# Kernel tuning notes

Measured on AMD Instinct MI355X. Metric: run time of the kernel, lower is better.

The kernel has to match this reference:

```python
import jax, jax.numpy as jnp
import numpy as np

E = 16      # num_experts
K = 2       # top-k
C = 1280    # capacity = ceil(8192*2/16*1.25)


def setup_inputs() -> dict:
    key = jax.random.key(0)
    ks = jax.random.split(key, 7)
    B, T, D, F, DFF = 4, 2048, 1024, 512, 512
    s = 0.02
    return {
        "hidden_state": jax.random.normal(ks[0], (B, T, D), jnp.float32),
        "router_w": jax.random.normal(ks[1], (D, E), jnp.float32) * s,
        "shared_gate_w": jax.random.normal(ks[2], (D, 1), jnp.float32) * s,
        "w1": jax.random.normal(ks[3], (E, D, F), jnp.float32) * s,
        "w2": jax.random.normal(ks[4], (E, F, D), jnp.float32) * s,
        "sw1": jax.random.normal(ks[5], (D, DFF), jnp.float32) * s,
        "sw2": jax.random.normal(ks[6], (DFF, D), jnp.float32) * s,
    }


def reference(hidden_state, router_w, shared_gate_w, w1, w2, sw1, sw2):
    B, T, D = hidden_state.shape
    N = B * T
    # Router: softmax over expert logits + shared sigmoid gate
    logits = jnp.einsum("btd,de->bte", hidden_state, router_w)
    scores = jax.nn.softmax(logits, axis=-1)                      # [B,T,E]
    g_shared = jax.nn.sigmoid(jnp.einsum("btd,do->bto", hidden_state, shared_gate_w))

    topk_vals, topk_idx = jax.lax.top_k(scores, K)                # [B,T,K]
    x = hidden_state.reshape(N, D)
    token_for_route = jnp.repeat(jnp.arange(N), K)                # [N*K]
    expert_for_route = topk_idx.reshape(-1)                       # [N*K]
    gate_for_route = topk_vals.reshape(-1)                        # [N*K]

    # Stable sort by expert (jnp.argsort is stable)
    order = jnp.argsort(expert_for_route)
    expert_sorted = expert_for_route[order]
    token_sorted = token_for_route[order]
    gate_sorted = gate_for_route[order]
    x_sorted = x[token_sorted]                                    # [N*K, D]

    counts = jnp.bincount(expert_sorted, length=E)
    starts = jnp.cumsum(counts) - counts
    r = jnp.arange(N * K)
    positions = r - starts[expert_sorted]                         # slot within expert
    keep = (positions < C) & (gate_sorted != 0)
    p_idx = jnp.clip(positions, 0, C - 1)

    # Scatter kept tokens into fixed-capacity buffers; dropped routes go to dummy row E
    e_safe = jnp.where(keep, expert_sorted, E)
    p_safe = jnp.where(keep, p_idx, 0)
    buf = jnp.zeros((E + 1, C, D), x.dtype).at[e_safe, p_safe].set(
        jnp.where(keep[:, None], x_sorted, 0.0)
    )
    expert_inputs = buf[:E]                                       # [E,C,D]

    # Batched expert FFN (exact GELU, matching torch default)
    h = jax.nn.gelu(jnp.einsum("ech,ehf->ecf", expert_inputs, w1), approximate=False)
    expert_outputs = jnp.einsum("ecf,efh->ech", h, w2)            # [E,C,D]

    gate_eff = jnp.where(keep, gate_sorted, 0.0)
    y_sorted = expert_outputs[expert_sorted, p_idx] * gate_eff[:, None]

    # Combine: scatter-add back to tokens
    y_out = jnp.zeros((N, D), x.dtype).at[token_sorted].add(y_sorted).reshape(B, T, D)

    # Shared expert path
    shared_out = (jax.nn.gelu(x @ sw1, approximate=False) @ sw2).reshape(B, T, D)
    y_out = y_out + g_shared * shared_out

    # Stats (no attention_mask path)
    load_counts = jnp.bincount(expert_for_route, length=E)
    load = load_counts / (load_counts.sum() + 1e-12)
    importance = scores.mean(axis=(0, 1))
    return (y_out, importance, load)
```

## Files before the change

kernel.cpp:

```cpp
#include <hip/hip_runtime.h>
#include <hip/hip_bf16.h>
#include <math.h>

#define N_TOK 8192
#define DIM 1024
#define NEXP 16
#define CAP 1280
#define FDIM 512
#define NROUTE (N_TOK * 2)
#define NCHUNK 64
#define ECAP (NEXP * CAP)
#define TOTROW (ECAP + N_TOK)

typedef __hip_bfloat16 bf16;
typedef unsigned short ushort_t;
typedef __attribute__((ext_vector_type(8))) short bf16x8;
typedef __attribute__((ext_vector_type(4))) float f32x4;

__device__ __forceinline__ float gelu_fast(float x) {
    float u = 1.5957691216057308f * (x + 0.044715f * x * x * x);
    return x / (1.f + __expf(-u));
}

__device__ __forceinline__ float bf2f(unsigned short u) {
    union { float f; unsigned int i; } v; v.i = ((unsigned int)u) << 16; return v.f;
}

__device__ __forceinline__ unsigned short f2b(float f) {
    union { __hip_bfloat16 h; unsigned short u; } v;
    v.h = __float2bfloat16(f);
    return v.u;
}

__device__ __forceinline__ void gload16(const void* g, void* l) {
    __builtin_amdgcn_global_load_lds(
        (const __attribute__((address_space(1))) unsigned int*)g,
        (__attribute__((address_space(3))) unsigned int*)l,
        16, 0, 0);
}

__device__ __forceinline__ int swz_addr16(int r, int q) {
    return ((r >> 1) << 3) + ((r & 1) << 2) + (q ^ ((r >> 1) & 3));
}

__global__ __launch_bounds__(256) void gather_x_kernel(
    const ushort_t* __restrict__ x_bf, const int* __restrict__ slot_token,
    const int* __restrict__ counts_cap, ushort_t* __restrict__ xg)
{
    int row = blockIdx.x;
    int e = row / CAP;
    int pos = row - e * CAP;
    int tok = (pos < counts_cap[e]) ? slot_token[row] : 0;
    if ((unsigned)tok >= N_TOK) tok = 0;
    int c = threadIdx.x * 4;
    ushort4 v = *reinterpret_cast<const ushort4*>(x_bf + (size_t)tok * DIM + c);
    *reinterpret_cast<ushort4*>(xg + (size_t)row * DIM + c) = v;
}

#define PREP_RTR_BLOCKS 512
#define PREP_NWG (PREP_RTR_BLOCKS + 1088)
__global__ __launch_bounds__(256) void prep_kernel(
    const float* __restrict__ x, const float* __restrict__ rw,
    const float* __restrict__ sgw,
    const float* __restrict__ w1, const float* __restrict__ w2,
    const float* __restrict__ sw1, const float* __restrict__ sw2,
    float* __restrict__ scores,
    int* __restrict__ topk_idx,
    float* __restrict__ topk_val,
    float* __restrict__ g_shared,
    ushort_t* __restrict__ x_bf,
    ushort_t* __restrict__ w1t, ushort_t* __restrict__ w2t,
    ushort_t* __restrict__ sw1t, ushort_t* __restrict__ sw2t)
{
    __shared__ union {
        ushort_t tileB[128][130];
        struct {
            float acc[4][16][4][4];
            float g[4][16];
        } r;
    } sm;

    if (blockIdx.x < PREP_RTR_BLOCKS) {
        int tid = threadIdx.x;
        int w = tid >> 6;
        int lane = tid & 63;
        int tok0 = blockIdx.x * 16;

        {
            int dq = w * 256 + lane * 4;
            float4 gv = *reinterpret_cast<const float4*>(sgw + dq);
#pragma unroll 4
            for (int tt = 0; tt < 16; ++tt) {
                const float* xr = x + (size_t)(tok0 + tt) * DIM + dq;
                float4 xv = *reinterpret_cast<const float4*>(xr);
                ushort4 o;
                o.x = f2b(xv.x); o.y = f2b(xv.y); o.z = f2b(xv.z); o.w = f2b(xv.w);
                *reinterpret_cast<ushort4*>(x_bf + (size_t)(tok0 + tt) * DIM + dq) = o;
                float dg = xv.x * gv.x + xv.y * gv.y + xv.z * gv.z + xv.w * gv.w;
#pragma unroll
                for (int m = 1; m < 64; m <<= 1) dg += __shfl_xor(dg, m, 64);
                if (lane == 0) sm.r.g[w][tt] = dg;
            }
        }

        int tok = lane >> 2;
        int e4 = lane & 3;
        int token = tok0 + tok;
        {
            const float* xr = x + (size_t)token * DIM + w * 256;
            const float* rwb = rw + (size_t)(w * 256) * NEXP + e4 * 4;
            float4 a0 = {0,0,0,0}, a1 = {0,0,0,0}, a2 = {0,0,0,0}, a3 = {0,0,0,0};
#pragma unroll 4
            for (int i = 0; i < 64; ++i) {
                float4 xv = *reinterpret_cast<const float4*>(xr + i * 4);
                const float* rp = rwb + (size_t)i * 4 * NEXP;
                float4 w0 = *reinterpret_cast<const float4*>(rp);
                float4 w1v = *reinterpret_cast<const float4*>(rp + NEXP);
                float4 w2v = *reinterpret_cast<const float4*>(rp + 2 * NEXP);
                float4 w3v = *reinterpret_cast<const float4*>(rp + 3 * NEXP);
                a0.x += xv.x * w0.x;  a0.y += xv.x * w0.y;  a0.z += xv.x * w0.z;  a0.w += xv.x * w0.w;
                a1.x += xv.y * w1v.x; a1.y += xv.y * w1v.y; a1.z += xv.y * w1v.z; a1.w += xv.y * w1v.w;
                a2.x += xv.z * w2v.x; a2.y += xv.z * w2v.y; a2.z += xv.z * w2v.z; a2.w += xv.z * w2v.w;
                a3.x += xv.w * w3v.x; a3.y += xv.w * w3v.y; a3.z += xv.w * w3v.z; a3.w += xv.w * w3v.w;
            }
            sm.r.acc[w][tok][e4][0] = (a0.x + a1.x) + (a2.x + a3.x);
            sm.r.acc[w][tok][e4][1] = (a0.y + a1.y) + (a2.y + a3.y);
            sm.r.acc[w][tok][e4][2] = (a0.z + a1.z) + (a2.z + a3.z);
            sm.r.acc[w][tok][e4][3] = (a0.w + a1.w) + (a2.w + a3.w);
        }
        __syncthreads();

        if (w != 0) return;

        float L0 = sm.r.acc[0][tok][e4][0] + sm.r.acc[1][tok][e4][0]
                 + sm.r.acc[2][tok][e4][0] + sm.r.acc[3][tok][e4][0];
        float L1 = sm.r.acc[0][tok][e4][1] + sm.r.acc[1][tok][e4][1]
                 + sm.r.acc[2][tok][e4][1] + sm.r.acc[3][tok][e4][1];
        float L2 = sm.r.acc[0][tok][e4][2] + sm.r.acc[1][tok][e4][2]
                 + sm.r.acc[2][tok][e4][2] + sm.r.acc[3][tok][e4][2];
        float L3 = sm.r.acc[0][tok][e4][3] + sm.r.acc[1][tok][e4][3]
                 + sm.r.acc[2][tok][e4][3] + sm.r.acc[3][tok][e4][3];

        float mx = fmaxf(fmaxf(L0, L1), fmaxf(L2, L3));
        mx = fmaxf(mx, __shfl_xor(mx, 1, 4));
        mx = fmaxf(mx, __shfl_xor(mx, 2, 4));
        float P0 = expf(L0 - mx), P1 = expf(L1 - mx);
        float P2 = expf(L2 - mx), P3 = expf(L3 - mx);
        float s = (P0 + P1) + (P2 + P3);
        s += __shfl_xor(s, 1, 4);
        s += __shfl_xor(s, 2, 4);
        float inv = 1.f / s;
        P0 *= inv; P1 *= inv; P2 *= inv; P3 *= inv;

        float4 Pv = {P0, P1, P2, P3};
        *reinterpret_cast<float4*>(scores + (size_t)token * NEXP + e4 * 4) = Pv;

        int base = e4 * 4;
        float v = P0; int idx = base;
        if (P1 > v) { v = P1; idx = base + 1; }
        if (P2 > v) { v = P2; idx = base + 2; }
        if (P3 > v) { v = P3; idx = base + 3; }
#pragma unroll
        for (int m = 1; m < 4; m <<= 1) {
            float vo = __shfl_xor(v, m, 4);
            int io = __shfl_xor(idx, m, 4);
            if (vo > v || (vo == v && io < idx)) { v = vo; idx = io; }
        }
        int i0 = idx; float v0 = v;
        float q0 = (base + 0 == i0) ? -1.f : P0;
        float q1 = (base + 1 == i0) ? -1.f : P1;
        float q2 = (base + 2 == i0) ? -1.f : P2;
        float q3 = (base + 3 == i0) ? -1.f : P3;
        v = q0; idx = base;
        if (q1 > v) { v = q1; idx = base + 1; }
        if (q2 > v) { v = q2; idx = base + 2; }
        if (q3 > v) { v = q3; idx = base + 3; }
#pragma unroll
        for (int m = 1; m < 4; m <<= 1) {
            float vo = __shfl_xor(v, m, 4);
            int io = __shfl_xor(idx, m, 4);
            if (vo > v || (vo == v && io < idx)) { v = vo; idx = io; }
        }
        if (e4 == 0) {
            topk_idx[2 * token] = i0; topk_idx[2 * token + 1] = idx;
            topk_val[2 * token] = v0; topk_val[2 * token + 1] = v;
            float ag = (sm.r.g[0][tok] + sm.r.g[1][tok]) + (sm.r.g[2][tok] + sm.r.g[3][tok]);
            g_shared[token] = 1.f / (1.f + expf(-ag));
        }
        return;
    }

    int bx = blockIdx.x - PREP_RTR_BLOCKS;
    const float* src; ushort_t* dst; int K, N, kt, nt;
    if (bx < 512) {
        int e = bx >> 5, r = bx & 31;
        K = 1024; N = 512; kt = r >> 2; nt = r & 3;
        src = w1 + (size_t)e * K * N; dst = w1t + (size_t)e * K * N;
    } else if (bx < 1024) {
        int b2 = bx - 512, e = b2 >> 5, r = b2 & 31;
        K = 512; N = 1024; kt = r >> 3; nt = r & 7;
        src = w2 + (size_t)e * K * N; dst = w2t + (size_t)e * K * N;
    } else if (bx < 1056) {
        int r = bx - 1024;
        K = 1024; N = 512; kt = r >> 2; nt = r & 3;
        src = sw1; dst = sw1t;
    } else {
        int r = bx - 1056;
        K = 512; N = 1024; kt = r >> 3; nt = r & 7;
        src = sw2; dst = sw2t;
    }
    int t = threadIdx.x;
#pragma unroll 4
    for (int i = 0; i < 16; ++i) {
        int u = t + 256 * i;
        int r = u >> 5;
        int c4 = (u & 31) * 4;
        float4 v = *reinterpret_cast<const float4*>(
            src + (size_t)(kt * 128 + r) * N + nt * 128 + c4);
        sm.tileB[c4 + 0][r] = f2b(v.x);
        sm.tileB[c4 + 1][r] = f2b(v.y);
        sm.tileB[c4 + 2][r] = f2b(v.z);
        sm.tileB[c4 + 3][r] = f2b(v.w);
    }
    __syncthreads();
#pragma unroll 4
    for (int i2 = 0; i2 < 8; ++i2) {
        int u = t + 256 * i2;
        int n = u >> 4;
        int kc = (u & 15) * 8;
        bf16x8 o;
#pragma unroll
        for (int j = 0; j < 8; ++j) o[j] = (short)sm.tileB[n][kc + j];
        *reinterpret_cast<bf16x8*>(dst + (size_t)(nt * 128 + n) * K + kt * 128 + kc) = o;
    }
}

__global__ __launch_bounds__(256) void hist_kernel(
    const int* __restrict__ topk_idx, int* __restrict__ chunk_hist)
{
    __shared__ int h[NEXP];
    int tid = threadIdx.x;
    if (tid < NEXP) h[tid] = 0;
    __syncthreads();
    int r = blockIdx.x * 256 + tid;
    atomicAdd(&h[topk_idx[r]], 1);
    __syncthreads();
    if (tid < NEXP) chunk_hist[blockIdx.x * NEXP + tid] = h[tid];
}

__global__ __launch_bounds__(64) void scan_kernel(
    const int* __restrict__ chunk_hist, int* __restrict__ chunk_off,
    int* __restrict__ counts_cap, float* __restrict__ out_tail)
{
    int e = threadIdx.x;
    if (e >= NEXP) return;
    int run = 0;
    for (int b = 0; b < NCHUNK; ++b) {
        chunk_off[b * NEXP + e] = run;
        run += chunk_hist[b * NEXP + e];
    }
    counts_cap[e] = run < CAP ? run : CAP;
    out_tail[NEXP + e] = (float)((double)run / 16384.0);
}

__global__ __launch_bounds__(256) void assign_kernel(
    const int* __restrict__ topk_idx, const float* __restrict__ topk_val,
    const int* __restrict__ chunk_off,
    int* __restrict__ route_slot, int* __restrict__ slot_token)
{
    __shared__ int wave_cnt[4][NEXP];
    int tid = threadIdx.x;
    int lane = tid & 63;
    int w = tid >> 6;
    int r = blockIdx.x * 256 + tid;
    int e = topk_idx[r];
    float gate = topk_val[r];
    int rank_w = 0;
#pragma unroll
    for (int e16 = 0; e16 < NEXP; ++e16) {
        unsigned long long bal = __ballot(e == e16);
        if (e == e16) rank_w = __popcll(bal & ((1ull << lane) - 1ull));
        if (lane == 0) wave_cnt[w][e16] = __popcll(bal);
    }
    __syncthreads();
    int rank = rank_w;
#pragma unroll
    for (int w2 = 0; w2 < 3; ++w2)
        if (w2 < w) rank += wave_cnt[w2][e];
    int pos = chunk_off[blockIdx.x * NEXP + e] + rank;
    int slot = -1;
    if (pos < CAP && gate != 0.f) {
        slot = e * CAP + pos;
        slot_token[slot] = r >> 1;
    }
    route_slot[r] = slot;
}

__global__ __launch_bounds__(256) void importance_kernel(
    const float* __restrict__ scores, float* __restrict__ out_tail)
{
    __shared__ float red[256];
    int e = blockIdx.x;
    float s = 0.f;
    for (int t = threadIdx.x; t < N_TOK; t += 256) s += scores[t * NEXP + e];
    red[threadIdx.x] = s;
    __syncthreads();
    for (int st = 128; st > 0; st >>= 1) {
        if (threadIdx.x < st) red[threadIdx.x] += red[threadIdx.x + st];
        __syncthreads();
    }
    if (threadIdx.x == 0) out_tail[e] = red[0] / (float)N_TOK;
}

#define G1_GX (NEXP * 5 + N_TOK / 256)
#define G1_NWG (G1_GX * (FDIM / 128))
__global__ __launch_bounds__(512) void gemm1_mfma(
    const ushort_t* __restrict__ xg,
    const ushort_t* __restrict__ x_bf,
    const ushort_t* __restrict__ w1t,
    const ushort_t* __restrict__ sw1t,
    const int* __restrict__ counts_cap,
    ushort_t* __restrict__ h_buf)
{
    __shared__ ushort_t As[3][256 * 32];
    __shared__ ushort_t Bs[3][128 * 32];

    int flat = blockIdx.x;
    int wg = (flat & 7) * (G1_NWG / 8) + (flat >> 3);
    int by = wg & 3;
    int bxg = wg >> 2;

    int g, rb;
    if (bxg < NEXP * 5) { g = bxg / 5; rb = bxg % 5; }
    else { g = NEXP; rb = bxg - NEXP * 5; }
    int Mg = (g < NEXP) ? counts_cap[g] : N_TOK;
    int m0 = rb * 256;
    if (m0 >= Mg) return;
    const ushort_t* Arows = (g < NEXP) ? (xg + ((size_t)g * CAP + m0) * DIM)
                                       : (x_bf + (size_t)m0 * DIM);
    const ushort_t* Bt = (g < NEXP) ? (w1t + (size_t)g * DIM * FDIM) : sw1t;
    int n0 = by * 128;
    int t = threadIdx.x;

    const ushort_t* asrc[2];
    const ushort_t* bsrc;
#pragma unroll
    for (int i = 0; i < 2; ++i) {
        int s = t + i * 512;
        int lr = ((s >> 3) << 1) | ((s >> 2) & 1);
        int qq = (s & 3) ^ ((s >> 3) & 3);
        asrc[i] = Arows + (size_t)lr * DIM + qq * 8;
    }
    {
        int s = t;
        int lr = ((s >> 3) << 1) | ((s >> 2) & 1);
        int qq = (s & 3) ^ ((s >> 3) & 3);
        bsrc = Bt + (size_t)(n0 + lr) * DIM + qq * 8;
    }

    int lane = t & 63;
    int w = t >> 6;
    int wm = (w & 3) * 64, wn = (w >> 2) * 64;
    int l15 = lane & 15, q = lane >> 4;

    int aoff[4], boff[4];
#pragma unroll
    for (int m = 0; m < 4; ++m) aoff[m] = swz_addr16(wm + m * 16 + l15, q) << 3;
#pragma unroll
    for (int n = 0; n < 4; ++n) boff[n] = swz_addr16(wn + n * 16 + l15, q) << 3;

    f32x4 acc[4][4];
#pragma unroll
    for (int m = 0; m < 4; ++m)
#pragma unroll
        for (int n = 0; n < 4; ++n) acc[m][n] = (f32x4){0.f, 0.f, 0.f, 0.f};

    auto STAGE = [&](int buf, int koff) {
        gload16(asrc[0] + koff, &As[buf][t * 8]);
        gload16(asrc[1] + koff, &As[buf][t * 8 + 4096]);
        gload16(bsrc + koff, &Bs[buf][t * 8]);
    };

    const int NSTEP = DIM / 32;
    STAGE(0, 0);
    STAGE(1, 32);
    asm volatile("s_waitcnt vmcnt(3)" ::: "memory");
    __builtin_amdgcn_s_barrier();
    asm volatile("" ::: "memory");

    int cur = 0, b2 = 2;
    for (int kt = 0; kt < NSTEP; ++kt) {
        if (kt + 2 < NSTEP) STAGE(b2, (kt + 2) * 32);
        const ushort_t* asb = &As[cur][0];
        const ushort_t* bsb = &Bs[cur][0];
        bf16x8 af[4], bfr[4];
#pragma unroll
        for (int m = 0; m < 4; ++m)
            af[m] = *reinterpret_cast<const bf16x8*>(asb + aoff[m]);
#pragma unroll
        for (int n = 0; n < 4; ++n)
            bfr[n] = *reinterpret_cast<const bf16x8*>(bsb + boff[n]);
        __builtin_amdgcn_s_setprio(1);
#pragma unroll
        for (int m = 0; m < 4; ++m)
#pragma unroll
            for (int n = 0; n < 4; ++n)
                acc[m][n] = __builtin_amdgcn_mfma_f32_16x16x32_bf16(
                    af[m], bfr[n], acc[m][n], 0, 0, 0);
        __builtin_amdgcn_s_setprio(0);
        if (kt + 1 < NSTEP) {
            if (kt + 2 < NSTEP) asm volatile("s_waitcnt vmcnt(3)" ::: "memory");
            else                asm volatile("s_waitcnt vmcnt(0)" ::: "memory");
            __builtin_amdgcn_s_barrier();
            asm volatile("" ::: "memory");
        }
        cur = (cur == 2) ? 0 : cur + 1;
        b2  = (b2 == 2) ? 0 : b2 + 1;
    }

    size_t obase = ((g < NEXP) ? (size_t)g * CAP : (size_t)ECAP) + m0;
#pragma unroll
    for (int m = 0; m < 4; ++m) {
#pragma unroll
        for (int r = 0; r < 4; ++r) {
            int grow = wm + m * 16 + q * 4 + r;
            ushort_t* orow = h_buf + (obase + grow) * FDIM + n0 + wn + l15;
#pragma unroll
            for (int n = 0; n < 4; ++n)
                orow[n * 16] = f2b(gelu_fast(acc[m][n][r]));
        }
    }
}

#define G2_NWG (G1_GX * (DIM / 128))
__global__ __launch_bounds__(512) void gemm2_mfma(
    const ushort_t* __restrict__ h_buf,
    const ushort_t* __restrict__ w2t,
    const ushort_t* __restrict__ sw2t,
    const int* __restrict__ counts_cap,
    const float* __restrict__ g_shared,
    ushort_t* __restrict__ out_buf,
    ushort_t* __restrict__ sh_out)
{
    __shared__ ushort_t As[2][256 * 32];
    __shared__ ushort_t Bs[2][128 * 32];

    int flat = blockIdx.x;
    int wg = (flat & 7) * (G2_NWG / 8) + (flat >> 3);
    int by = wg & 7;
    int bxg = wg >> 3;

    int g, rb;
    if (bxg < NEXP * 5) { g = bxg / 5; rb = bxg % 5; }
    else { g = NEXP; rb = bxg - NEXP * 5; }
    int Mg = (g < NEXP) ? counts_cap[g] : N_TOK;
    int m0 = rb * 256;
    if (m0 >= Mg) return;
    size_t abase = ((g < NEXP) ? (size_t)g * CAP : (size_t)ECAP) + m0;
    const ushort_t* Bt = (g < NEXP) ? (w2t + (size_t)g * FDIM * DIM) : sw2t;
    int n0 = by * 128;
    int t = threadIdx.x;

    const ushort_t* asrc[2];
    const ushort_t* bsrc;
#pragma unroll
    for (int i = 0; i < 2; ++i) {
        int s = t + i * 512;
        int lr = ((s >> 3) << 1) | ((s >> 2) & 1);
        int qq = (s & 3) ^ ((s >> 3) & 3);
        asrc[i] = h_buf + (abase + lr) * FDIM + qq * 8;
    }
    {
        int s = t;
        int lr = ((s >> 3) << 1) | ((s >> 2) & 1);
        int qq = (s & 3) ^ ((s >> 3) & 3);
        bsrc = Bt + (size_t)(n0 + lr) * FDIM + qq * 8;
    }

    int lane = t & 63;
    int w = t >> 6;
    int wm = (w & 3) * 64, wn = (w >> 2) * 64;
    int l15 = lane & 15, q = lane >> 4;

    int aoff[4], boff[4];
#pragma unroll
    for (int m = 0; m < 4; ++m) aoff[m] = swz_addr16(wm + m * 16 + l15, q) << 3;
#pragma unroll
    for (int n = 0; n < 4; ++n) boff[n] = swz_addr16(wn + n * 16 + l15, q) << 3;

    f32x4 acc[4][4];
#pragma unroll
    for (int m = 0; m < 4; ++m)
#pragma unroll
        for (int n = 0; n < 4; ++n) acc[m][n] = (f32x4){0.f, 0.f, 0.f, 0.f};

    auto STAGE = [&](int buf, int koff) {
        gload16(asrc[0] + koff, &As[buf][t * 8]);
        gload16(asrc[1] + koff, &As[buf][t * 8 + 4096]);
        gload16(bsrc + koff, &Bs[buf][t * 8]);
    };

    const int NSTEP = FDIM / 32;
    STAGE(0, 0);
    __syncthreads();

    int cur = 0;
    for (int kt = 0; kt < NSTEP; ++kt) {
        if (kt + 1 < NSTEP) STAGE(cur ^ 1, (kt + 1) * 32);
        const ushort_t* asb = &As[cur][0];
        const ushort_t* bsb = &Bs[cur][0];
        bf16x8 af[4], bfr[4];
#pragma unroll
        for (int m = 0; m < 4; ++m)
            af[m] = *reinterpret_cast<const bf16x8*>(asb + aoff[m]);
#pragma unroll
        for (int n = 0; n < 4; ++n)
            bfr[n] = *reinterpret_cast<const bf16x8*>(bsb + boff[n]);
        __builtin_amdgcn_s_setprio(1);
#pragma unroll
        for (int m = 0; m < 4; ++m)
#pragma unroll
            for (int n = 0; n < 4; ++n)
                acc[m][n] = __builtin_amdgcn_mfma_f32_16x16x32_bf16(
                    af[m], bfr[n], acc[m][n], 0, 0, 0);
        __builtin_amdgcn_s_setprio(0);
        __syncthreads();
        cur ^= 1;
    }

    if (g < NEXP) {
#pragma unroll
        for (int m = 0; m < 4; ++m) {
#pragma unroll
            for (int r = 0; r < 4; ++r) {
                int grow = wm + m * 16 + q * 4 + r;
                ushort_t* orow = out_buf + (abase + grow) * DIM + n0 + wn + l15;
#pragma unroll
                for (int n = 0; n < 4; ++n)
                    orow[n * 16] = f2b(acc[m][n][r]);
            }
        }
    } else {
#pragma unroll
        for (int m = 0; m < 4; ++m) {
#pragma unroll
            for (int r = 0; r < 4; ++r) {
                int tok = m0 + wm + m * 16 + q * 4 + r;
                float gs = g_shared[tok];
                ushort_t* orow = sh_out + (size_t)tok * DIM + n0 + wn + l15;
#pragma unroll
                for (int n = 0; n < 4; ++n)
                    orow[n * 16] = f2b(gs * acc[m][n][r]);
            }
        }
    }
}

__global__ __launch_bounds__(256) void combine_kernel(
    const ushort_t* __restrict__ out_buf, const ushort_t* __restrict__ sh_out,
    const int* __restrict__ route_slot, const float* __restrict__ topk_val,
    float* __restrict__ y)
{
    int token = blockIdx.x;
    int c = threadIdx.x * 4;
    ushort4 sv = *reinterpret_cast<const ushort4*>(sh_out + (size_t)token * DIM + c);
    float y0 = bf2f(sv.x), y1 = bf2f(sv.y), y2 = bf2f(sv.z), y3 = bf2f(sv.w);
#pragma unroll
    for (int k = 0; k < 2; ++k) {
        int s = route_slot[2 * token + k];
        if (s >= 0) {
            float gate = topk_val[2 * token + k];
            ushort4 rv = *reinterpret_cast<const ushort4*>(out_buf + (size_t)s * DIM + c);
            y0 += gate * bf2f(rv.x); y1 += gate * bf2f(rv.y);
            y2 += gate * bf2f(rv.z); y3 += gate * bf2f(rv.w);
        }
    }
    float4 o; o.x = y0; o.y = y1; o.z = y2; o.w = y3;
    *reinterpret_cast<float4*>(y + (size_t)token * DIM + c) = o;
}

extern "C" void kernel_launch(void* const* d_in, const int* in_sizes, int n_in,
                              void* d_out, int out_size, void* d_ws, size_t ws_size,
                              hipStream_t stream) {
    const float* x   = (const float*)d_in[0];
    const float* rw  = (const float*)d_in[1];
    const float* sgw = (const float*)d_in[2];
    const float* w1  = (const float*)d_in[3];
    const float* w2  = (const float*)d_in[4];
    const float* sw1 = (const float*)d_in[5];
    const float* sw2 = (const float*)d_in[6];
    float* y = (float*)d_out;
    float* out_tail = y + (size_t)N_TOK * DIM;

    size_t off = 0;
    char* wsb = (char*)d_ws;
    auto alloc = [&](size_t bytes) -> void* {
        void* p = wsb + off;
        off += (bytes + 255) & ~(size_t)255;
        return p;
    };
    float*    scores     = (float*)alloc((size_t)N_TOK * NEXP * 4);
    int*      topk_idx   = (int*)alloc((size_t)NROUTE * 4);
    float*    topk_val   = (float*)alloc((size_t)NROUTE * 4);
    float*    g_shared   = (float*)alloc((size_t)N_TOK * 4);
    int*      chunk_hist = (int*)alloc((size_t)NCHUNK * NEXP * 4);
    int*      chunk_off  = (int*)alloc((size_t)NCHUNK * NEXP * 4);
    int*      counts_cap = (int*)alloc((size_t)NEXP * 4);
    int*      route_slot = (int*)alloc((size_t)NROUTE * 4);
    int*      slot_token = (int*)alloc((size_t)ECAP * 4);
    char*     xg_union   = (char*)alloc((size_t)ECAP * DIM * 2);
    ushort_t* xg         = (ushort_t*)xg_union;
    ushort_t* out_buf    = (ushort_t*)xg_union;
    ushort_t* x_bf       = (ushort_t*)alloc((size_t)N_TOK * DIM * 2);
    ushort_t* sh_out     = x_bf;
    ushort_t* w1t        = (ushort_t*)alloc((size_t)NEXP * DIM * FDIM * 2);
    ushort_t* w2t        = (ushort_t*)alloc((size_t)NEXP * DIM * FDIM * 2);
    ushort_t* sw1t       = (ushort_t*)alloc((size_t)DIM * FDIM * 2);
    ushort_t* sw2t       = (ushort_t*)alloc((size_t)DIM * FDIM * 2);
    ushort_t* h_buf      = (ushort_t*)alloc((size_t)TOTROW * FDIM * 2);
    (void)ws_size; (void)in_sizes; (void)n_in; (void)out_size;

    prep_kernel<<<PREP_NWG, 256, 0, stream>>>(
        x, rw, sgw, w1, w2, sw1, sw2,
        scores, topk_idx, topk_val, g_shared, x_bf, w1t, w2t, sw1t, sw2t);
    hist_kernel<<<NCHUNK, 256, 0, stream>>>(topk_idx, chunk_hist);
    scan_kernel<<<1, 64, 0, stream>>>(chunk_hist, chunk_off, counts_cap, out_tail);
    assign_kernel<<<NCHUNK, 256, 0, stream>>>(topk_idx, topk_val, chunk_off, route_slot, slot_token);
    importance_kernel<<<NEXP, 256, 0, stream>>>(scores, out_tail);
    gather_x_kernel<<<ECAP, 256, 0, stream>>>(x_bf, slot_token, counts_cap, xg);

    gemm1_mfma<<<G1_NWG, 512, 0, stream>>>(xg, x_bf, w1t, sw1t, counts_cap, h_buf);
    gemm2_mfma<<<G2_NWG, 512, 0, stream>>>(h_buf, w2t, sw2t, counts_cap, g_shared, out_buf, sh_out);

    combine_kernel<<<N_TOK, 256, 0, stream>>>(out_buf, sh_out, route_slot, topk_val, y);
}
```

Measured before the change: 174.2 us.

## Stage router token rows in LDS and halve tokens per router block

Router blocks now handle 8 tokens instead of 16, doubling the router grid. Each token row is staged into shared memory during the bf16 conversion pass, and the router dot products then read x from LDS instead of global memory. The reduction dimension is split across two lanes per token, which are combined with a shuffle. This trades a second global read of x for LDS reads and adds parallelism, at the cost of a larger shared footprint (about 33KB) that may reduce occupancy of the prep kernel.

```diff
diff --git a/kernel.cpp b/kernel.cpp
--- a/kernel.cpp
+++ b/kernel.cpp
@@ -57,7 +57,7 @@
     *reinterpret_cast<ushort4*>(xg + (size_t)row * DIM + c) = v;
 }
 
-#define PREP_RTR_BLOCKS 512
+#define PREP_RTR_BLOCKS 1024
 #define PREP_NWG (PREP_RTR_BLOCKS + 1088)
 __global__ __launch_bounds__(256) void prep_kernel(
     const float* __restrict__ x, const float* __restrict__ rw,
@@ -75,8 +75,9 @@
     __shared__ union {
         ushort_t tileB[128][130];
         struct {
-            float acc[4][16][4][4];
-            float g[4][16];
+            float xl[8][1028];
+            float racc[4][8][4][4];
+            float g[4][8];
         } r;
     } sm;
 
@@ -84,15 +85,16 @@
         int tid = threadIdx.x;
         int w = tid >> 6;
         int lane = tid & 63;
-        int tok0 = blockIdx.x * 16;
+        int tok0 = blockIdx.x * 8;
 
         {
             int dq = w * 256 + lane * 4;
             float4 gv = *reinterpret_cast<const float4*>(sgw + dq);
-#pragma unroll 4
-            for (int tt = 0; tt < 16; ++tt) {
+#pragma unroll
+            for (int tt = 0; tt < 8; ++tt) {
                 const float* xr = x + (size_t)(tok0 + tt) * DIM + dq;
                 float4 xv = *reinterpret_cast<const float4*>(xr);
+                *reinterpret_cast<float4*>(&sm.r.xl[tt][dq]) = xv;
                 ushort4 o;
                 o.x = f2b(xv.x); o.y = f2b(xv.y); o.z = f2b(xv.z); o.w = f2b(xv.w);
                 *reinterpret_cast<ushort4*>(x_bf + (size_t)(tok0 + tt) * DIM + dq) = o;
@@ -102,17 +104,18 @@
                 if (lane == 0) sm.r.g[w][tt] = dg;
             }
         }
-
-        int tok = lane >> 2;
+        __syncthreads();
+
+        int tok = lane >> 3;
+        int dup = (lane >> 2) & 1;
         int e4 = lane & 3;
-        int token = tok0 + tok;
         {
-            const float* xr = x + (size_t)token * DIM + w * 256;
-            const float* rwb = rw + (size_t)(w * 256) * NEXP + e4 * 4;
+            int base_d = w * 256 + dup * 128;
+            const float* rwb = rw + (size_t)base_d * NEXP + e4 * 4;
             float4 a0 = {0,0,0,0}, a1 = {0,0,0,0}, a2 = {0,0,0,0}, a3 = {0,0,0,0};
 #pragma unroll 4
-            for (int i = 0; i < 64; ++i) {
-                float4 xv = *reinterpret_cast<const float4*>(xr + i * 4);
+            for (int i = 0; i < 32; ++i) {
+                float4 xv = *reinterpret_cast<const float4*>(&sm.r.xl[tok][base_d + i * 4]);
                 const float* rp = rwb + (size_t)i * 4 * NEXP;
                 float4 w0 = *reinterpret_cast<const float4*>(rp);
                 float4 w1v = *reinterpret_cast<const float4*>(rp + NEXP);
@@ -123,23 +126,35 @@
                 a2.x += xv.z * w2v.x; a2.y += xv.z * w2v.y; a2.z += xv.z * w2v.z; a2.w += xv.z * w2v.w;
                 a3.x += xv.w * w3v.x; a3.y += xv.w * w3v.y; a3.z += xv.w * w3v.z; a3.w += xv.w * w3v.w;
             }
-            sm.r.acc[w][tok][e4][0] = (a0.x + a1.x) + (a2.x + a3.x);
-            sm.r.acc[w][tok][e4][1] = (a0.y + a1.y) + (a2.y + a3.y);
-            sm.r.acc[w][tok][e4][2] = (a0.z + a1.z) + (a2.z + a3.z);
-            sm.r.acc[w][tok][e4][3] = (a0.w + a1.w) + (a2.w + a3.w);
+            float s0 = (a0.x + a1.x) + (a2.x + a3.x);
+            float s1 = (a0.y + a1.y) + (a2.y + a3.y);
+            float s2 = (a0.z + a1.z) + (a2.z + a3.z);
+            float s3 = (a0.w + a1.w) + (a2.w + a3.w);
+            s0 += __shfl_xor(s0, 4, 64);
+            s1 += __shfl_xor(s1, 4, 64);
+            s2 += __shfl_xor(s2, 4, 64);
+            s3 += __shfl_xor(s3, 4, 64);
+            if (dup == 0) {
+                sm.r.racc[w][tok][e4][0] = s0;
+                sm.r.racc[w][tok][e4][1] = s1;
+                sm.r.racc[w][tok][e4][2] = s2;
+                sm.r.racc[w][tok][e4][3] = s3;
+            }
         }
         __syncthreads();
 
-        if (w != 0) return;
-
-        float L0 = sm.r.acc[0][tok][e4][0] + sm.r.acc[1][tok][e4][0]
-                 + sm.r.acc[2][tok][e4][0] + sm.r.acc[3][tok][e4][0];
-        float L1 = sm.r.acc[0][tok][e4][1] + sm.r.acc[1][tok][e4][1]
-                 + sm.r.acc[2][tok][e4][1] + sm.r.acc[3][tok][e4][1];
-        float L2 = sm.r.acc[0][tok][e4][2] + sm.r.acc[1][tok][e4][2]
-                 + sm.r.acc[2][tok][e4][2] + sm.r.acc[3][tok][e4][2];
-        float L3 = sm.r.acc[0][tok][e4][3] + sm.r.acc[1][tok][e4][3]
-                 + sm.r.acc[2][tok][e4][3] + sm.r.acc[3][tok][e4][3];
+        if (tid >= 32) return;
+        int tk = tid >> 2;
+        int eq = tid & 3;
+        int token = tok0 + tk;
+        float L0 = sm.r.racc[0][tk][eq][0] + sm.r.racc[1][tk][eq][0]
+                 + sm.r.racc[2][tk][eq][0] + sm.r.racc[3][tk][eq][0];
+        float L1 = sm.r.racc[0][tk][eq][1] + sm.r.racc[1][tk][eq][1]
+                 + sm.r.racc[2][tk][eq][1] + sm.r.racc[3][tk][eq][1];
+        float L2 = sm.r.racc[0][tk][eq][2] + sm.r.racc[1][tk][eq][2]
+                 + sm.r.racc[2][tk][eq][2] + sm.r.racc[3][tk][eq][2];
+        float L3 = sm.r.racc[0][tk][eq][3] + sm.r.racc[1][tk][eq][3]
+                 + sm.r.racc[2][tk][eq][3] + sm.r.racc[3][tk][eq][3];
 
         float mx = fmaxf(fmaxf(L0, L1), fmaxf(L2, L3));
         mx = fmaxf(mx, __shfl_xor(mx, 1, 4));
@@ -153,9 +168,9 @@
         P0 *= inv; P1 *= inv; P2 *= inv; P3 *= inv;
 
         float4 Pv = {P0, P1, P2, P3};
-        *reinterpret_cast<float4*>(scores + (size_t)token * NEXP + e4 * 4) = Pv;
-
-        int base = e4 * 4;
+        *reinterpret_cast<float4*>(scores + (size_t)token * NEXP + eq * 4) = Pv;
+
+        int base = eq * 4;
         float v = P0; int idx = base;
         if (P1 > v) { v = P1; idx = base + 1; }
         if (P2 > v) { v = P2; idx = base + 2; }
@@ -181,10 +196,10 @@
             int io = __shfl_xor(idx, m, 4);
             if (vo > v || (vo == v && io < idx)) { v = vo; idx = io; }
         }
-        if (e4 == 0) {
+        if (eq == 0) {
             topk_idx[2 * token] = i0; topk_idx[2 * token + 1] = idx;
             topk_val[2 * token] = v0; topk_val[2 * token + 1] = v;
-            float ag = (sm.r.g[0][tok] + sm.r.g[1][tok]) + (sm.r.g[2][tok] + sm.r.g[3][tok]);
+            float ag = (sm.r.g[0][tk] + sm.r.g[1][tk]) + (sm.r.g[2][tk] + sm.r.g[3][tk]);
             g_shared[token] = 1.f / (1.f + expf(-ag));
         }
         return;
```

New measurement: 167.0 us. 4.1% less time.
